# Optimization experiments

Measured on AMD Instinct MI355X. Metric: run time of the kernel, lower is better.

The kernel has to match this reference:

```python
import jax, jax.numpy as jnp
import numpy as np

B, T, D, H = 128, 256, 64, 512
MISSING = 128.0  # MISSING_VALUE marker from AJ-RNN repo


def _lstm_params(key, in_dim):
    k1, k2 = jax.random.split(key)
    K = jax.random.normal(k1, (in_dim, 4 * H), jnp.float32) * 0.05
    R = jax.random.normal(k2, (H, 4 * H), jnp.float32) * 0.05
    # Keras LSTMCell: zeros bias with unit forget bias (gate order i, f, c, o)
    b = jnp.concatenate([jnp.zeros((H,)), jnp.ones((H,)), jnp.zeros((2 * H,))]).astype(jnp.float32)
    return K, R, b


def setup_inputs() -> dict:
    key = jax.random.key(0)
    ks = jax.random.split(key, 6)
    x = jax.random.normal(ks[0], (B, T, D), jnp.float32)
    miss = jax.random.uniform(ks[1], (B, T, D)) < 0.2
    x = jnp.where(miss, MISSING, x)  # inject missing-value markers
    k0, r0, b0 = _lstm_params(ks[2], D)   # layer 0: input dim D
    k1, r1, b1 = _lstm_params(ks[3], H)   # layer 1: input dim H
    W = jax.random.normal(ks[4], (H, D), jnp.float32) * 0.1  # imputation kernel
    bias = jnp.full((D,), 0.1, jnp.float32)
    return dict(x=x, k0=k0, r0=r0, b0=b0, k1=k1, r1=r1, b1=b1, W=W, bias=bias)


def _lstm_cell(x, h, c, K, R, b):
    z = x @ K + h @ R + b  # [B, 4H]
    i, f, g, o = jnp.split(z, 4, axis=-1)
    i = jax.nn.sigmoid(i)
    f = jax.nn.sigmoid(f)
    g = jnp.tanh(g)
    o = jax.nn.sigmoid(o)
    c_new = f * c + i * g
    h_new = o * jnp.tanh(c_new)
    return h_new, c_new


def reference(x, k0, r0, b0, k1, r1, b1, W, bias):
    xs = jnp.swapaxes(x, 0, 1)          # [T, B, D]
    flags = jnp.arange(T) > 0           # t==0 uses raw input, no imputation

    def step(carry, inp):
        h1, c1, h2, c2 = carry
        x_t, flag = inp
        pred = h2 @ W + bias            # prediction from previous top-layer output
        cur = jnp.where(flag & (x_t == MISSING), pred, x_t)
        h1, c1 = _lstm_cell(cur, h1, c1, k0, r0, b0)
        h2, c2 = _lstm_cell(h1, h2, c2, k1, r1, b1)
        return (h1, c1, h2, c2), h2

    init = tuple(jnp.zeros((B, H), jnp.float32) for _ in range(4))
    _, outs = jax.lax.scan(step, init, (xs, flags))  # outs: [T, B, H]

    # tf.concat(outputs[:-1], axis=1) then reshape [-1, H] == batch-major, time inner
    hidden = jnp.swapaxes(outs[:-1], 0, 1).reshape(-1, H)  # [B*(T-1), H]
    prediction = hidden @ W + bias                          # [B*(T-1), D]
    last_cell = outs[-1]                                    # [B, H]
    return prediction, last_cell
```

## Files before the change

### kernel.cpp

```cpp
#include <hip/hip_runtime.h>
#include <hip/hip_bf16.h>


typedef __bf16        v8bf  __attribute__((ext_vector_type(8)));
typedef float         f32x4 __attribute__((ext_vector_type(4)));
typedef unsigned int  u32x4 __attribute__((ext_vector_type(4)));

constexpr int B_ = 128, T_ = 256, D_ = 64, H_ = 512;

constexpr size_t OFF_WP1 = 0;
constexpr size_t OFF_WP2 = 2359296;
constexpr size_t OFF_WPP = 6553600;
constexpr size_t OFF_H1G = 6619136;
constexpr size_t OFF_H2G = 6750208;
constexpr size_t OFF_FLG = 6881280;

__device__ __forceinline__ v8bf ldv(const __hip_bfloat16* p) {
  return *reinterpret_cast<const v8bf*>(p);
}
__device__ __forceinline__ f32x4 MF(v8bf a, v8bf b, f32x4 c) {
  return __builtin_amdgcn_mfma_f32_16x16x32_bf16(a, b, c, 0, 0, 0);
}
__device__ __forceinline__ float sigf(float x) { return 1.0f / (1.0f + __expf(-x)); }
__device__ __forceinline__ float tanhfast(float x) {
  x = fminf(15.0f, fmaxf(-15.0f, x));
  float e = __expf(-2.0f * x);
  return (1.0f - e) / (1.0f + e);
}

__device__ __forceinline__ void st_llc_u16(void* p, unsigned v) {
  asm volatile("global_store_short %0, %1, off sc0 sc1" :: "v"(p), "v"(v) : "memory");
}
__device__ __forceinline__ void vm0() {
  asm volatile("s_waitcnt vmcnt(0)" ::: "memory");
}
__device__ __forceinline__ void ld_llc64_issue(const char* g, u32x4& a, u32x4& b,
                                               u32x4& c, u32x4& d) {
  asm volatile(
      "global_load_dwordx4 %0, %4, off sc0 sc1\n\t"
      "global_load_dwordx4 %1, %4, off offset:16 sc0 sc1\n\t"
      "global_load_dwordx4 %2, %4, off offset:32 sc0 sc1\n\t"
      "global_load_dwordx4 %3, %4, off offset:48 sc0 sc1"
      : "=&v"(a), "=&v"(b), "=&v"(c), "=&v"(d)
      : "v"(g)
      : "memory");
}

__global__ __launch_bounds__(256) void pack_weights(
    const float* __restrict__ kp, const float* __restrict__ rp,
    int krows, int ncols, int nkc, int nct, __hip_bfloat16* __restrict__ out) {
  int tid = blockIdx.x * 256 + threadIdx.x;
  int total = nct * nkc * 64;
  if (tid >= total) return;
  int L  = tid & 63;
  int kc = (tid >> 6) % nkc;
  int ct = tid / (64 * nkc);
  int n  = ct * 16 + (L & 15);
  int kb = kc * 32 + (L >> 4) * 8;
  __hip_bfloat16* dst = out + (size_t)tid * 8;
#pragma unroll
  for (int j = 0; j < 8; ++j) {
    int kk = kb + j;
    float v = (kk < krows) ? kp[kk * ncols + n] : rp[(kk - krows) * ncols + n];
    dst[j] = __float2bfloat16(v);
  }
}

__global__ __launch_bounds__(256) void init_state(unsigned* __restrict__ flg) {
  int idx = blockIdx.x * 256 + threadIdx.x;
  if (idx < 512) flg[idx] = 0u;
}

__global__ __launch_bounds__(256, 1) void rnn_persist(
    const float* __restrict__ x,
    const __hip_bfloat16* __restrict__ Wp1,
    const __hip_bfloat16* __restrict__ Wp2,
    const __hip_bfloat16* __restrict__ WpP,
    const float* __restrict__ b0,
    const float* __restrict__ b1,
    const float* __restrict__ biasD,
    __hip_bfloat16* __restrict__ h1g,
    __hip_bfloat16* __restrict__ h2g,
    unsigned* __restrict__ flg,
    float* __restrict__ pred_out,
    float* __restrict__ last_out) {

  __shared__ alignas(16) __hip_bfloat16 h1P[16][512];
  __shared__ alignas(16) __hip_bfloat16 h1Q[16][512];
  __shared__ alignas(16) __hip_bfloat16 h2L[16][512];
  __shared__ alignas(16) __hip_bfloat16 curL[16][72];
  __shared__ alignas(16) float predb[16][68];
  __shared__ float zb[4][16][17];

  const int tid = threadIdx.x;
  const int rg = blockIdx.x & 7;
  const int cg = blockIdx.x >> 3;
  const int w  = tid >> 6;
  const int L  = tid & 63;
  const int m  = L & 15;
  const int q  = L >> 4;
  const int row2 = tid >> 4;
  const int col2 = tid & 15;
  const int C  = cg * 16 + col2;
  const int R  = rg * 16 + row2;
  const int c0 = col2 * 4;
  const int sw = (m & 7) << 3;

  const int so0 = col2 * 64;
  const int ssw = (row2 & 7) << 4;
  const size_t gso = (size_t)row2 * 1024 + so0;

  v8bf wpp[16], wp1[18], wp2[32];
  {
    const int ct = w * 32 + cg;
#pragma unroll
    for (int kc = 0; kc < 16; ++kc)
      wpp[kc] = ldv(WpP + ((size_t)(w * 16 + kc) * 64 + L) * 8);
#pragma unroll
    for (int kc = 0; kc < 18; ++kc)
      wp1[kc] = ldv(Wp1 + ((size_t)(ct * 18 + kc) * 64 + L) * 8);
#pragma unroll
    for (int kc = 0; kc < 32; ++kc)
      wp2[kc] = ldv(Wp2 + ((size_t)(ct * 32 + kc) * 64 + L) * 8);
  }
  const float b0i = b0[C], b0f = b0[512 + C], b0g = b0[1024 + C], b0o = b0[1536 + C];
  const float b1i = b1[C], b1f = b1[512 + C], b1g = b1[1024 + C], b1o = b1[1536 + C];
  const float bD  = biasD[w * 16 + m];

  float c1v = 0.0f, c2v = 0.0f;

  const size_t rgbase = (size_t)rg * 16 * H_;
  const float* xrow = x + (size_t)R * T_ * D_;
  float* prow = pred_out + (size_t)R * (T_ - 1) * D_;
  unsigned* cnt = flg + rg * 64;
  const int hidx = R * H_ + C;

  {
    u32x4 zz = {0u, 0u, 0u, 0u};
    u32x4* p1 = reinterpret_cast<u32x4*>(&h1P[0][0]);
    u32x4* p2 = reinterpret_cast<u32x4*>(&h2L[0][0]);
#pragma unroll
    for (int i = 0; i < 4; ++i) { p1[tid * 4 + i] = zz; p2[tid * 4 + i] = zz; }
  }
  __syncthreads();

  f32x4 z1a = {0.f,0.f,0.f,0.f}, z1b = {0.f,0.f,0.f,0.f};

  for (int t = 0; t < T_; ++t) {
    __hip_bfloat16 (*h1L)[512] = (t & 1) ? h1Q : h1P;
    __hip_bfloat16 (*h1N)[512] = (t & 1) ? h1P : h1Q;

    const float4 xv = *reinterpret_cast<const float4*>(xrow + t * D_ + c0);

#pragma unroll
    for (int c = 8; c < 12; c += 2) {
      v8bf a0 = ldv(&h1L[m][(c * 32 + q * 8) ^ sw]);
      v8bf a1 = ldv(&h1L[m][((c + 1) * 32 + q * 8) ^ sw]);
      z1a = MF(a0, wp1[2 + c], z1a);
      z1b = MF(a1, wp1[3 + c], z1b);
    }
    if (t > 0 && tid < 64) {
      const unsigned tgt = 64u * (unsigned)t;
      while (__hip_atomic_load(cnt, __ATOMIC_RELAXED, __HIP_MEMORY_SCOPE_AGENT) < tgt)
        __builtin_amdgcn_s_sleep(1);
    }
    __syncthreads();

    u32x4 sa, sb, sc2, sd;
    if (t > 0)
      ld_llc64_issue((const char*)(h2g + rgbase) + gso, sa, sb, sc2, sd);
#pragma unroll
    for (int c = 12; c < 16; c += 2) {
      v8bf a0 = ldv(&h1L[m][(c * 32 + q * 8) ^ sw]);
      v8bf a1 = ldv(&h1L[m][((c + 1) * 32 + q * 8) ^ sw]);
      z1a = MF(a0, wp1[2 + c], z1a);
      z1b = MF(a1, wp1[3 + c], z1b);
    }
    if (t > 0) {
      vm0();
      char* lb = (char*)(&h2L[row2][0]);
      *(u32x4*)(lb + ((so0 +  0) ^ ssw)) = sa;
      *(u32x4*)(lb + ((so0 + 16) ^ ssw)) = sb;
      *(u32x4*)(lb + ((so0 + 32) ^ ssw)) = sc2;
      *(u32x4*)(lb + ((so0 + 48) ^ ssw)) = sd;
    }
    __syncthreads();

    if (t > 0) {
      f32x4 a0 = {0.f,0.f,0.f,0.f}, a1 = {0.f,0.f,0.f,0.f};
#pragma unroll
      for (int kc = 0; kc < 16; kc += 2) {
        v8bf x0 = ldv(&h2L[m][(kc * 32 + q * 8) ^ sw]);
        v8bf x1 = ldv(&h2L[m][((kc + 1) * 32 + q * 8) ^ sw]);
        a0 = MF(x0, wpp[kc], a0);
        a1 = MF(x1, wpp[kc + 1], a1);
      }
      a0 += a1;
#pragma unroll
      for (int r = 0; r < 4; ++r) predb[q * 4 + r][w * 16 + m] = a0[r] + bD;
    }
    __syncthreads();

    {
      float4 pv = {0.f, 0.f, 0.f, 0.f};
      if (t > 0) pv = *reinterpret_cast<const float4*>(&predb[row2][c0]);
      const float xa[4] = {xv.x, xv.y, xv.z, xv.w};
      const float pa[4] = {pv.x, pv.y, pv.z, pv.w};
#pragma unroll
      for (int j = 0; j < 4; ++j) {
        const bool missv = (t > 0) && (xa[j] == 128.0f);
        curL[row2][c0 + j] = __float2bfloat16(missv ? pa[j] : xa[j]);
      }
      if (cg == 0 && t > 0)
        *reinterpret_cast<float4*>(prow + (size_t)(t - 1) * D_ + c0) = pv;
    }
    __syncthreads();

    {
      v8bf a0 = ldv(&curL[m][q * 8]);
      v8bf a1 = ldv(&curL[m][32 + q * 8]);
      z1a = MF(a0, wp1[0], z1a);
      z1b = MF(a1, wp1[1], z1b);
      f32x4 zf = z1a + z1b;
#pragma unroll
      for (int r = 0; r < 4; ++r) zb[w][q * 4 + r][m] = zf[r];
    }
    __syncthreads();

    f32x4 z2a = {0.f,0.f,0.f,0.f}, z2b = {0.f,0.f,0.f,0.f};
    {
      float iv = zb[0][row2][col2] + b0i;
      float fv = zb[1][row2][col2] + b0f;
      float gv = zb[2][row2][col2] + b0g;
      float ov = zb[3][row2][col2] + b0o;
      float ig = sigf(iv), fg = sigf(fv), gg = tanhfast(gv), og = sigf(ov);
      c1v = fg * c1v + ig * gg;
      float hn = og * tanhfast(c1v);
      st_llc_u16(&h1g[hidx], (unsigned)__builtin_bit_cast(unsigned short,
                                                          __float2bfloat16(hn)));
    }
#pragma unroll
    for (int c = 0; c < 8; c += 2) {
      v8bf a0 = ldv(&h2L[m][(c * 32 + q * 8) ^ sw]);
      v8bf a1 = ldv(&h2L[m][((c + 1) * 32 + q * 8) ^ sw]);
      z2a = MF(a0, wp2[16 + c], z2a);
      z2b = MF(a1, wp2[17 + c], z2b);
    }
    vm0();
    __syncthreads();
    if (tid == 0)
      __hip_atomic_fetch_add(cnt, 1u, __ATOMIC_RELAXED, __HIP_MEMORY_SCOPE_AGENT);

#pragma unroll
    for (int c = 8; c < 12; c += 2) {
      v8bf a0 = ldv(&h2L[m][(c * 32 + q * 8) ^ sw]);
      v8bf a1 = ldv(&h2L[m][((c + 1) * 32 + q * 8) ^ sw]);
      z2a = MF(a0, wp2[16 + c], z2a);
      z2b = MF(a1, wp2[17 + c], z2b);
    }
    if (tid < 64) {
      const unsigned tgt = 32u * (2u * (unsigned)t + 1u);
      while (__hip_atomic_load(cnt, __ATOMIC_RELAXED, __HIP_MEMORY_SCOPE_AGENT) < tgt)
        __builtin_amdgcn_s_sleep(1);
    }
    __syncthreads();

    ld_llc64_issue((const char*)(h1g + rgbase) + gso, sa, sb, sc2, sd);
#pragma unroll
    for (int c = 12; c < 16; c += 2) {
      v8bf a0 = ldv(&h2L[m][(c * 32 + q * 8) ^ sw]);
      v8bf a1 = ldv(&h2L[m][((c + 1) * 32 + q * 8) ^ sw]);
      z2a = MF(a0, wp2[16 + c], z2a);
      z2b = MF(a1, wp2[17 + c], z2b);
    }
    vm0();
    {
      char* lb = (char*)(&h1N[row2][0]);
      *(u32x4*)(lb + ((so0 +  0) ^ ssw)) = sa;
      *(u32x4*)(lb + ((so0 + 16) ^ ssw)) = sb;
      *(u32x4*)(lb + ((so0 + 32) ^ ssw)) = sc2;
      *(u32x4*)(lb + ((so0 + 48) ^ ssw)) = sd;
    }
    __syncthreads();

    {
#pragma unroll
      for (int c = 0; c < 16; c += 2) {
        v8bf a0 = ldv(&h1N[m][(c * 32 + q * 8) ^ sw]);
        v8bf a1 = ldv(&h1N[m][((c + 1) * 32 + q * 8) ^ sw]);
        z2a = MF(a0, wp2[c], z2a);
        z2b = MF(a1, wp2[c + 1], z2b);
      }
      f32x4 zf = z2a + z2b;
#pragma unroll
      for (int r = 0; r < 4; ++r) zb[w][q * 4 + r][m] = zf[r];
    }
    __syncthreads();

    {
      float iv = zb[0][row2][col2] + b1i;
      float fv = zb[1][row2][col2] + b1f;
      float gv = zb[2][row2][col2] + b1g;
      float ov = zb[3][row2][col2] + b1o;
      float ig = sigf(iv), fg = sigf(fv), gg = tanhfast(gv), og = sigf(ov);
      c2v = fg * c2v + ig * gg;
      float hn = og * tanhfast(c2v);
      if (t == T_ - 1) {
        last_out[hidx] = hn;
        break;
      }
      st_llc_u16(&h2g[hidx], (unsigned)__builtin_bit_cast(unsigned short,
                                                          __float2bfloat16(hn)));
    }
    z1a = (f32x4){0.f,0.f,0.f,0.f};
    z1b = (f32x4){0.f,0.f,0.f,0.f};
#pragma unroll
    for (int c = 0; c < 8; c += 2) {
      v8bf a0 = ldv(&h1N[m][(c * 32 + q * 8) ^ sw]);
      v8bf a1 = ldv(&h1N[m][((c + 1) * 32 + q * 8) ^ sw]);
      z1a = MF(a0, wp1[2 + c], z1a);
      z1b = MF(a1, wp1[3 + c], z1b);
    }
    vm0();
    __syncthreads();
    if (tid == 0)
      __hip_atomic_fetch_add(cnt, 1u, __ATOMIC_RELAXED, __HIP_MEMORY_SCOPE_AGENT);
  }
}

extern "C" void kernel_launch(void* const* d_in, const int* in_sizes, int n_in,
                              void* d_out, int out_size, void* d_ws, size_t ws_size,
                              hipStream_t stream) {
  const float* x    = (const float*)d_in[0];
  const float* k0   = (const float*)d_in[1];
  const float* r0   = (const float*)d_in[2];
  const float* b0   = (const float*)d_in[3];
  const float* k1   = (const float*)d_in[4];
  const float* r1   = (const float*)d_in[5];
  const float* b1   = (const float*)d_in[6];
  const float* W    = (const float*)d_in[7];
  const float* bias = (const float*)d_in[8];

  char* ws = (char*)d_ws;
  __hip_bfloat16* Wp1 = (__hip_bfloat16*)(ws + OFF_WP1);
  __hip_bfloat16* Wp2 = (__hip_bfloat16*)(ws + OFF_WP2);
  __hip_bfloat16* WpP = (__hip_bfloat16*)(ws + OFF_WPP);
  __hip_bfloat16* h1g = (__hip_bfloat16*)(ws + OFF_H1G);
  __hip_bfloat16* h2g = (__hip_bfloat16*)(ws + OFF_H2G);
  unsigned*       flg = (unsigned*)(ws + OFF_FLG);

  pack_weights<<<(128 * 18 * 64 + 255) / 256, 256, 0, stream>>>(k0, r0, 64, 2048, 18, 128, Wp1);
  pack_weights<<<(128 * 32 * 64 + 255) / 256, 256, 0, stream>>>(k1, r1, 512, 2048, 32, 128, Wp2);
  pack_weights<<<(4 * 16 * 64 + 255) / 256, 256, 0, stream>>>(W, W, 512, 64, 16, 4, WpP);
  init_state<<<2, 256, 0, stream>>>(flg);

  float* outp = (float*)d_out;
  float* last = outp + (size_t)B_ * (T_ - 1) * D_;

  rnn_persist<<<256, 256, 0, stream>>>(x, Wp1, Wp2, WpP, b0, b1, bias,
                                       h1g, h2g, flg, outp, last);
}
```

Baseline: 1.467 ms.

## Interleave two batch row-groups per block to hide inter-block sync latency

```diff
diff --git a/kernel.cpp b/kernel.cpp
--- a/kernel.cpp
+++ b/kernel.cpp
@@ -69,6 +69,198 @@
 __global__ __launch_bounds__(256) void init_state(unsigned* __restrict__ flg) {
   int idx = blockIdx.x * 256 + threadIdx.x;
   if (idx < 512) flg[idx] = 0u;
+}
+
+struct TC {
+  int tid, cg, w, m, q, row2, col2, c0, sw, so0, ssw;
+  size_t gso;
+};
+
+__device__ __forceinline__ void half1(
+    int t, const TC& tc,
+    __hip_bfloat16 (*h1L)[512], __hip_bfloat16 (*h2L)[512],
+    __hip_bfloat16 (*curL)[72], float (*predb)[68], float (*zb)[16][17],
+    unsigned* cnt, const float* xrow, float* prow,
+    const char* h2src, __hip_bfloat16* h1dst,
+    const v8bf (&wpp)[16], const v8bf (&wp1)[18],
+    float b0i, float b0f, float b0g, float b0o, float bD,
+    float& c1v) {
+  const int tid = tc.tid, m = tc.m, q = tc.q, w = tc.w;
+  const int row2 = tc.row2, col2 = tc.col2, c0 = tc.c0, sw = tc.sw;
+  const int so0 = tc.so0, ssw = tc.ssw;
+  f32x4 z1a = {0.f,0.f,0.f,0.f}, z1b = {0.f,0.f,0.f,0.f};
+  const float4 xv = *reinterpret_cast<const float4*>(xrow + t * D_ + c0);
+
+  if (t > 0) {
+    if (tid < 64) {
+      const unsigned tgt = 64u * (unsigned)t;
+      while (__hip_atomic_load(cnt, __ATOMIC_RELAXED, __HIP_MEMORY_SCOPE_AGENT) < tgt)
+        __builtin_amdgcn_s_sleep(1);
+    }
+    __syncthreads();
+    u32x4 sa, sb, sc2, sd;
+    ld_llc64_issue(h2src + tc.gso, sa, sb, sc2, sd);
+#pragma unroll
+    for (int c = 0; c < 8; c += 2) {
+      v8bf a0 = ldv(&h1L[m][(c * 32 + q * 8) ^ sw]);
+      v8bf a1 = ldv(&h1L[m][((c + 1) * 32 + q * 8) ^ sw]);
+      z1a = MF(a0, wp1[2 + c], z1a);
+      z1b = MF(a1, wp1[3 + c], z1b);
+    }
+    vm0();
+    {
+      char* lb = (char*)(&h2L[row2][0]);
+      *(u32x4*)(lb + ((so0 +  0) ^ ssw)) = sa;
+      *(u32x4*)(lb + ((so0 + 16) ^ ssw)) = sb;
+      *(u32x4*)(lb + ((so0 + 32) ^ ssw)) = sc2;
+      *(u32x4*)(lb + ((so0 + 48) ^ ssw)) = sd;
+    }
+    __syncthreads();
+    {
+      f32x4 a0 = {0.f,0.f,0.f,0.f}, a1 = {0.f,0.f,0.f,0.f};
+#pragma unroll
+      for (int kc = 0; kc < 16; kc += 2) {
+        v8bf x0 = ldv(&h2L[m][(kc * 32 + q * 8) ^ sw]);
+        v8bf x1 = ldv(&h2L[m][((kc + 1) * 32 + q * 8) ^ sw]);
+        a0 = MF(x0, wpp[kc], a0);
+        a1 = MF(x1, wpp[kc + 1], a1);
+      }
+      a0 += a1;
+#pragma unroll
+      for (int r = 0; r < 4; ++r) predb[q * 4 + r][w * 16 + m] = a0[r] + bD;
+    }
+    __syncthreads();
+  }
+
+  {
+    float4 pv = {0.f, 0.f, 0.f, 0.f};
+    if (t > 0) pv = *reinterpret_cast<const float4*>(&predb[row2][c0]);
+    const float xa[4] = {xv.x, xv.y, xv.z, xv.w};
+    const float pa[4] = {pv.x, pv.y, pv.z, pv.w};
+#pragma unroll
+    for (int j = 0; j < 4; ++j) {
+      const bool missv = (t > 0) && (xa[j] == 128.0f);
+      curL[row2][c0 + j] = __float2bfloat16(missv ? pa[j] : xa[j]);
+    }
+    if (tc.cg == 0 && t > 0)
+      *reinterpret_cast<float4*>(prow + (size_t)(t - 1) * D_ + c0) = pv;
+  }
+  __syncthreads();
+
+  {
+#pragma unroll
+    for (int c = 8; c < 16; c += 2) {
+      v8bf a0 = ldv(&h1L[m][(c * 32 + q * 8) ^ sw]);
+      v8bf a1 = ldv(&h1L[m][((c + 1) * 32 + q * 8) ^ sw]);
+      z1a = MF(a0, wp1[2 + c], z1a);
+      z1b = MF(a1, wp1[3 + c], z1b);
+    }
+    v8bf a0 = ldv(&curL[m][q * 8]);
+    v8bf a1 = ldv(&curL[m][32 + q * 8]);
+    z1a = MF(a0, wp1[0], z1a);
+    z1b = MF(a1, wp1[1], z1b);
+    f32x4 zf = z1a + z1b;
+#pragma unroll
+    for (int r = 0; r < 4; ++r) zb[w][q * 4 + r][m] = zf[r];
+  }
+  __syncthreads();
+
+  {
+    float iv = zb[0][row2][col2] + b0i;
+    float fv = zb[1][row2][col2] + b0f;
+    float gv = zb[2][row2][col2] + b0g;
+    float ov = zb[3][row2][col2] + b0o;
+    float ig = sigf(iv), fg = sigf(fv), gg = tanhfast(gv), og = sigf(ov);
+    c1v = fg * c1v + ig * gg;
+    float hn = og * tanhfast(c1v);
+    st_llc_u16(h1dst, (unsigned)__builtin_bit_cast(unsigned short,
+                                                   __float2bfloat16(hn)));
+  }
+  vm0();
+  __syncthreads();
+  if (tid == 0)
+    __hip_atomic_fetch_add(cnt, 1u, __ATOMIC_RELAXED, __HIP_MEMORY_SCOPE_AGENT);
+}
+
+__device__ __forceinline__ void half2(
+    int t, const TC& tc,
+    __hip_bfloat16 (*h1N)[512], __hip_bfloat16 (*h2L)[512],
+    float (*zb)[16][17],
+    unsigned* cnt, const char* h1src,
+    __hip_bfloat16* h2dst, float* lastp,
+    const v8bf (&wp2)[32],
+    float b1i, float b1f, float b1g, float b1o,
+    float& c2v) {
+  const int tid = tc.tid, m = tc.m, q = tc.q, w = tc.w;
+  const int row2 = tc.row2, col2 = tc.col2, sw = tc.sw;
+  const int so0 = tc.so0, ssw = tc.ssw;
+  f32x4 z2a = {0.f,0.f,0.f,0.f}, z2b = {0.f,0.f,0.f,0.f};
+
+#pragma unroll
+  for (int c = 0; c < 8; c += 2) {
+    v8bf a0 = ldv(&h2L[m][(c * 32 + q * 8) ^ sw]);
+    v8bf a1 = ldv(&h2L[m][((c + 1) * 32 + q * 8) ^ sw]);
+    z2a = MF(a0, wp2[16 + c], z2a);
+    z2b = MF(a1, wp2[17 + c], z2b);
+  }
+  if (tid < 64) {
+    const unsigned tgt = 32u * (2u * (unsigned)t + 1u);
+    while (__hip_atomic_load(cnt, __ATOMIC_RELAXED, __HIP_MEMORY_SCOPE_AGENT) < tgt)
+      __builtin_amdgcn_s_sleep(1);
+  }
+  __syncthreads();
+  {
+    u32x4 sa, sb, sc2, sd;
+    ld_llc64_issue(h1src + tc.gso, sa, sb, sc2, sd);
+#pragma unroll
+    for (int c = 8; c < 16; c += 2) {
+      v8bf a0 = ldv(&h2L[m][(c * 32 + q * 8) ^ sw]);
+      v8bf a1 = ldv(&h2L[m][((c + 1) * 32 + q * 8) ^ sw]);
+      z2a = MF(a0, wp2[16 + c], z2a);
+      z2b = MF(a1, wp2[17 + c], z2b);
+    }
+    vm0();
+    char* lb = (char*)(&h1N[row2][0]);
+    *(u32x4*)(lb + ((so0 +  0) ^ ssw)) = sa;
+    *(u32x4*)(lb + ((so0 + 16) ^ ssw)) = sb;
+    *(u32x4*)(lb + ((so0 + 32) ^ ssw)) = sc2;
+    *(u32x4*)(lb + ((so0 + 48) ^ ssw)) = sd;
+  }
+  __syncthreads();
+  {
+#pragma unroll
+    for (int c = 0; c < 16; c += 2) {
+      v8bf a0 = ldv(&h1N[m][(c * 32 + q * 8) ^ sw]);
+      v8bf a1 = ldv(&h1N[m][((c + 1) * 32 + q * 8) ^ sw]);
+      z2a = MF(a0, wp2[c], z2a);
+      z2b = MF(a1, wp2[c + 1], z2b);
+    }
+    f32x4 zf = z2a + z2b;
+#pragma unroll
+    for (int r = 0; r < 4; ++r) zb[w][q * 4 + r][m] = zf[r];
+  }
+  __syncthreads();
+  {
+    float iv = zb[0][row2][col2] + b1i;
+    float fv = zb[1][row2][col2] + b1f;
+    float gv = zb[2][row2][col2] + b1g;
+    float ov = zb[3][row2][col2] + b1o;
+    float ig = sigf(iv), fg = sigf(fv), gg = tanhfast(gv), og = sigf(ov);
+    c2v = fg * c2v + ig * gg;
+    float hn = og * tanhfast(c2v);
+    if (t == T_ - 1) {
+      *lastp = hn;
+    } else {
+      st_llc_u16(h2dst, (unsigned)__builtin_bit_cast(unsigned short,
+                                                     __float2bfloat16(hn)));
+    }
+  }
+  if (t != T_ - 1) {
+    vm0();
+    __syncthreads();
+    if (tid == 0)
+      __hip_atomic_fetch_add(cnt, 1u, __ATOMIC_RELAXED, __HIP_MEMORY_SCOPE_AGENT);
+  }
 }
 
 __global__ __launch_bounds__(256, 1) void rnn_persist(
@@ -85,37 +277,38 @@
     float* __restrict__ pred_out,
     float* __restrict__ last_out) {
 
-  __shared__ alignas(16) __hip_bfloat16 h1P[16][512];
-  __shared__ alignas(16) __hip_bfloat16 h1Q[16][512];
-  __shared__ alignas(16) __hip_bfloat16 h2L[16][512];
-  __shared__ alignas(16) __hip_bfloat16 curL[16][72];
-  __shared__ alignas(16) float predb[16][68];
-  __shared__ float zb[4][16][17];
-
-  const int tid = threadIdx.x;
-  const int rg = blockIdx.x & 7;
-  const int cg = blockIdx.x >> 3;
-  const int w  = tid >> 6;
-  const int L  = tid & 63;
-  const int m  = L & 15;
-  const int q  = L >> 4;
-  const int row2 = tid >> 4;
-  const int col2 = tid & 15;
-  const int C  = cg * 16 + col2;
-  const int R  = rg * 16 + row2;
-  const int c0 = col2 * 4;
-  const int sw = (m & 7) << 3;
-
-  const int so0 = col2 * 64;
-  const int ssw = (row2 & 7) << 4;
-  const size_t gso = (size_t)row2 * 1024 + so0;
+  __shared__ alignas(16) __hip_bfloat16 h1PA[16][512], h1QA[16][512], h2LA[16][512];
+  __shared__ alignas(16) __hip_bfloat16 h1PB[16][512], h1QB[16][512], h2LB[16][512];
+  __shared__ alignas(16) __hip_bfloat16 curLA[16][72], curLB[16][72];
+  __shared__ alignas(16) float predbA[16][68], predbB[16][68];
+  __shared__ float zbA[4][16][17], zbB[4][16][17];
+
+  TC tc;
+  tc.tid  = threadIdx.x;
+  const int pr = blockIdx.x & 3;
+  tc.cg   = blockIdx.x >> 2;
+  tc.w    = tc.tid >> 6;
+  const int L = tc.tid & 63;
+  tc.m    = L & 15;
+  tc.q    = L >> 4;
+  tc.row2 = tc.tid >> 4;
+  tc.col2 = tc.tid & 15;
+  tc.c0   = tc.col2 * 4;
+  tc.sw   = (tc.m & 7) << 3;
+  tc.so0  = tc.col2 * 64;
+  tc.ssw  = (tc.row2 & 7) << 4;
+  tc.gso  = (size_t)tc.row2 * 1024 + tc.so0;
+
+  const int rgA = pr, rgB = pr + 4;
+  const int C = tc.cg * 16 + tc.col2;
+  const int RA = rgA * 16 + tc.row2, RB = rgB * 16 + tc.row2;
 
   v8bf wpp[16], wp1[18], wp2[32];
   {
-    const int ct = w * 32 + cg;
+    const int ct = tc.w * 32 + tc.cg;
 #pragma unroll
     for (int kc = 0; kc < 16; ++kc)
-      wpp[kc] = ldv(WpP + ((size_t)(w * 16 + kc) * 64 + L) * 8);
+      wpp[kc] = ldv(WpP + ((size_t)(tc.w * 16 + kc) * 64 + L) * 8);
 #pragma unroll
     for (int kc = 0; kc < 18; ++kc)
       wp1[kc] = ldv(Wp1 + ((size_t)(ct * 18 + kc) * 64 + L) * 8);
@@ -125,206 +318,51 @@
   }
   const float b0i = b0[C], b0f = b0[512 + C], b0g = b0[1024 + C], b0o = b0[1536 + C];
   const float b1i = b1[C], b1f = b1[512 + C], b1g = b1[1024 + C], b1o = b1[1536 + C];
-  const float bD  = biasD[w * 16 + m];
-
-  float c1v = 0.0f, c2v = 0.0f;
-
-  const size_t rgbase = (size_t)rg * 16 * H_;
-  const float* xrow = x + (size_t)R * T_ * D_;
-  float* prow = pred_out + (size_t)R * (T_ - 1) * D_;
-  unsigned* cnt = flg + rg * 64;
-  const int hidx = R * H_ + C;
+  const float bD  = biasD[tc.w * 16 + tc.m];
+
+  float c1A = 0.0f, c2A = 0.0f, c1B = 0.0f, c2B = 0.0f;
+
+  const size_t rgbaseA = (size_t)rgA * 16 * H_, rgbaseB = (size_t)rgB * 16 * H_;
+  const float* xrowA = x + (size_t)RA * T_ * D_;
+  const float* xrowB = x + (size_t)RB * T_ * D_;
+  float* prowA = pred_out + (size_t)RA * (T_ - 1) * D_;
+  float* prowB = pred_out + (size_t)RB * (T_ - 1) * D_;
+  unsigned* cntA = flg + rgA * 64;
+  unsigned* cntB = flg + rgB * 64;
+  const int hidxA = RA * H_ + C, hidxB = RB * H_ + C;
+  const char* h2srcA = (const char*)(h2g + rgbaseA);
+  const char* h2srcB = (const char*)(h2g + rgbaseB);
+  const char* h1srcA = (const char*)(h1g + rgbaseA);
+  const char* h1srcB = (const char*)(h1g + rgbaseB);
 
   {
     u32x4 zz = {0u, 0u, 0u, 0u};
-    u32x4* p1 = reinterpret_cast<u32x4*>(&h1P[0][0]);
-    u32x4* p2 = reinterpret_cast<u32x4*>(&h2L[0][0]);
-#pragma unroll
-    for (int i = 0; i < 4; ++i) { p1[tid * 4 + i] = zz; p2[tid * 4 + i] = zz; }
-  }
-  __syncthreads();
-
-  f32x4 z1a = {0.f,0.f,0.f,0.f}, z1b = {0.f,0.f,0.f,0.f};
+    u32x4* p1 = reinterpret_cast<u32x4*>(&h1PA[0][0]);
+    u32x4* p2 = reinterpret_cast<u32x4*>(&h2LA[0][0]);
+    u32x4* p3 = reinterpret_cast<u32x4*>(&h1PB[0][0]);
+    u32x4* p4 = reinterpret_cast<u32x4*>(&h2LB[0][0]);
+#pragma unroll
+    for (int i = 0; i < 4; ++i) {
+      p1[tc.tid * 4 + i] = zz; p2[tc.tid * 4 + i] = zz;
+      p3[tc.tid * 4 + i] = zz; p4[tc.tid * 4 + i] = zz;
+    }
+  }
+  __syncthreads();
 
   for (int t = 0; t < T_; ++t) {
-    __hip_bfloat16 (*h1L)[512] = (t & 1) ? h1Q : h1P;
-    __hip_bfloat16 (*h1N)[512] = (t & 1) ? h1P : h1Q;
-
-    const float4 xv = *reinterpret_cast<const float4*>(xrow + t * D_ + c0);
-
-#pragma unroll
-    for (int c = 8; c < 12; c += 2) {
-      v8bf a0 = ldv(&h1L[m][(c * 32 + q * 8) ^ sw]);
-      v8bf a1 = ldv(&h1L[m][((c + 1) * 32 + q * 8) ^ sw]);
-      z1a = MF(a0, wp1[2 + c], z1a);
-      z1b = MF(a1, wp1[3 + c], z1b);
-    }
-    if (t > 0 && tid < 64) {
-      const unsigned tgt = 64u * (unsigned)t;
-      while (__hip_atomic_load(cnt, __ATOMIC_RELAXED, __HIP_MEMORY_SCOPE_AGENT) < tgt)
-        __builtin_amdgcn_s_sleep(1);
-    }
-    __syncthreads();
-
-    u32x4 sa, sb, sc2, sd;
-    if (t > 0)
-      ld_llc64_issue((const char*)(h2g + rgbase) + gso, sa, sb, sc2, sd);
-#pragma unroll
-    for (int c = 12; c < 16; c += 2) {
-      v8bf a0 = ldv(&h1L[m][(c * 32 + q * 8) ^ sw]);
-      v8bf a1 = ldv(&h1L[m][((c + 1) * 32 + q * 8) ^ sw]);
-      z1a = MF(a0, wp1[2 + c], z1a);
-      z1b = MF(a1, wp1[3 + c], z1b);
-    }
-    if (t > 0) {
-      vm0();
-      char* lb = (char*)(&h2L[row2][0]);
-      *(u32x4*)(lb + ((so0 +  0) ^ ssw)) = sa;
-      *(u32x4*)(lb + ((so0 + 16) ^ ssw)) = sb;
-      *(u32x4*)(lb + ((so0 + 32) ^ ssw)) = sc2;
-      *(u32x4*)(lb + ((so0 + 48) ^ ssw)) = sd;
-    }
-    __syncthreads();
-
-    if (t > 0) {
-      f32x4 a0 = {0.f,0.f,0.f,0.f}, a1 = {0.f,0.f,0.f,0.f};
-#pragma unroll
-      for (int kc = 0; kc < 16; kc += 2) {
-        v8bf x0 = ldv(&h2L[m][(kc * 32 + q * 8) ^ sw]);
-        v8bf x1 = ldv(&h2L[m][((kc + 1) * 32 + q * 8) ^ sw]);
-        a0 = MF(x0, wpp[kc], a0);
-        a1 = MF(x1, wpp[kc + 1], a1);
-      }
-      a0 += a1;
-#pragma unroll
-      for (int r = 0; r < 4; ++r) predb[q * 4 + r][w * 16 + m] = a0[r] + bD;
-    }
-    __syncthreads();
-
-    {
-      float4 pv = {0.f, 0.f, 0.f, 0.f};
-      if (t > 0) pv = *reinterpret_cast<const float4*>(&predb[row2][c0]);
-      const float xa[4] = {xv.x, xv.y, xv.z, xv.w};
-      const float pa[4] = {pv.x, pv.y, pv.z, pv.w};
-#pragma unroll
-      for (int j = 0; j < 4; ++j) {
-        const bool missv = (t > 0) && (xa[j] == 128.0f);
-        curL[row2][c0 + j] = __float2bfloat16(missv ? pa[j] : xa[j]);
-      }
-      if (cg == 0 && t > 0)
-        *reinterpret_cast<float4*>(prow + (size_t)(t - 1) * D_ + c0) = pv;
-    }
-    __syncthreads();
-
-    {
-      v8bf a0 = ldv(&curL[m][q * 8]);
-      v8bf a1 = ldv(&curL[m][32 + q * 8]);
-      z1a = MF(a0, wp1[0], z1a);
-      z1b = MF(a1, wp1[1], z1b);
-      f32x4 zf = z1a + z1b;
-#pragma unroll
-      for (int r = 0; r < 4; ++r) zb[w][q * 4 + r][m] = zf[r];
-    }
-    __syncthreads();
-
-    f32x4 z2a = {0.f,0.f,0.f,0.f}, z2b = {0.f,0.f,0.f,0.f};
-    {
-      float iv = zb[0][row2][col2] + b0i;
-      float fv = zb[1][row2][col2] + b0f;
-      float gv = zb[2][row2][col2] + b0g;
-      float ov = zb[3][row2][col2] + b0o;
-      float ig = sigf(iv), fg = sigf(fv), gg = tanhfast(gv), og = sigf(ov);
-      c1v = fg * c1v + ig * gg;
-      float hn = og * tanhfast(c1v);
-      st_llc_u16(&h1g[hidx], (unsigned)__builtin_bit_cast(unsigned short,
-                                                          __float2bfloat16(hn)));
-    }
-#pragma unroll
-    for (int c = 0; c < 8; c += 2) {
-      v8bf a0 = ldv(&h2L[m][(c * 32 + q * 8) ^ sw]);
-      v8bf a1 = ldv(&h2L[m][((c + 1) * 32 + q * 8) ^ sw]);
-      z2a = MF(a0, wp2[16 + c], z2a);
-      z2b = MF(a1, wp2[17 + c], z2b);
-    }
-    vm0();
-    __syncthreads();
-    if (tid == 0)
-      __hip_atomic_fetch_add(cnt, 1u, __ATOMIC_RELAXED, __HIP_MEMORY_SCOPE_AGENT);
-
-#pragma unroll
-    for (int c = 8; c < 12; c += 2) {
-      v8bf a0 = ldv(&h2L[m][(c * 32 + q * 8) ^ sw]);
-      v8bf a1 = ldv(&h2L[m][((c + 1) * 32 + q * 8) ^ sw]);
-      z2a = MF(a0, wp2[16 + c], z2a);
-      z2b = MF(a1, wp2[17 + c], z2b);
-    }
-    if (tid < 64) {
-      const unsigned tgt = 32u * (2u * (unsigned)t + 1u);
-      while (__hip_atomic_load(cnt, __ATOMIC_RELAXED, __HIP_MEMORY_SCOPE_AGENT) < tgt)
-        __builtin_amdgcn_s_sleep(1);
-    }
-    __syncthreads();
-
-    ld_llc64_issue((const char*)(h1g + rgbase) + gso, sa, sb, sc2, sd);
-#pragma unroll
-    for (int c = 12; c < 16; c += 2) {
-      v8bf a0 = ldv(&h2L[m][(c * 32 + q * 8) ^ sw]);
-      v8bf a1 = ldv(&h2L[m][((c + 1) * 32 + q * 8) ^ sw]);
-      z2a = MF(a0, wp2[16 + c], z2a);
-      z2b = MF(a1, wp2[17 + c], z2b);
-    }
-    vm0();
-    {
-      char* lb = (char*)(&h1N[row2][0]);
-      *(u32x4*)(lb + ((so0 +  0) ^ ssw)) = sa;
-      *(u32x4*)(lb + ((so0 + 16) ^ ssw)) = sb;
-      *(u32x4*)(lb + ((so0 + 32) ^ ssw)) = sc2;
-      *(u32x4*)(lb + ((so0 + 48) ^ ssw)) = sd;
-    }
-    __syncthreads();
-
-    {
-#pragma unroll
-      for (int c = 0; c < 16; c += 2) {
-        v8bf a0 = ldv(&h1N[m][(c * 32 + q * 8) ^ sw]);
-        v8bf a1 = ldv(&h1N[m][((c + 1) * 32 + q * 8) ^ sw]);
-        z2a = MF(a0, wp2[c], z2a);
-        z2b = MF(a1, wp2[c + 1], z2b);
-      }
-      f32x4 zf = z2a + z2b;
-#pragma unroll
-      for (int r = 0; r < 4; ++r) zb[w][q * 4 + r][m] = zf[r];
-    }
-    __syncthreads();
-
-    {
-      float iv = zb[0][row2][col2] + b1i;
-      float fv = zb[1][row2][col2] + b1f;
-      float gv = zb[2][row2][col2] + b1g;
-      float ov = zb[3][row2][col2] + b1o;
-      float ig = sigf(iv), fg = sigf(fv), gg = tanhfast(gv), og = sigf(ov);
-      c2v = fg * c2v + ig * gg;
-      float hn = og * tanhfast(c2v);
-      if (t == T_ - 1) {
-        last_out[hidx] = hn;
-        break;
-      }
-      st_llc_u16(&h2g[hidx], (unsigned)__builtin_bit_cast(unsigned short,
-                                                          __float2bfloat16(hn)));
-    }
-    z1a = (f32x4){0.f,0.f,0.f,0.f};
-    z1b = (f32x4){0.f,0.f,0.f,0.f};
-#pragma unroll
-    for (int c = 0; c < 8; c += 2) {
-      v8bf a0 = ldv(&h1N[m][(c * 32 + q * 8) ^ sw]);
-      v8bf a1 = ldv(&h1N[m][((c + 1) * 32 + q * 8) ^ sw]);
-      z1a = MF(a0, wp1[2 + c], z1a);
-      z1b = MF(a1, wp1[3 + c], z1b);
-    }
-    vm0();
-    __syncthreads();
-    if (tid == 0)
-      __hip_atomic_fetch_add(cnt, 1u, __ATOMIC_RELAXED, __HIP_MEMORY_SCOPE_AGENT);
+    __hip_bfloat16 (*h1LA)[512] = (t & 1) ? h1QA : h1PA;
+    __hip_bfloat16 (*h1NA)[512] = (t & 1) ? h1PA : h1QA;
+    __hip_bfloat16 (*h1LB)[512] = (t & 1) ? h1QB : h1PB;
+    __hip_bfloat16 (*h1NB)[512] = (t & 1) ? h1PB : h1QB;
+
+    half1(t, tc, h1LA, h2LA, curLA, predbA, zbA, cntA, xrowA, prowA,
+          h2srcA, h1g + hidxA, wpp, wp1, b0i, b0f, b0g, b0o, bD, c1A);
+    half1(t, tc, h1LB, h2LB, curLB, predbB, zbB, cntB, xrowB, prowB,
+          h2srcB, h1g + hidxB, wpp, wp1, b0i, b0f, b0g, b0o, bD, c1B);
+    half2(t, tc, h1NA, h2LA, zbA, cntA, h1srcA,
+          h2g + hidxA, last_out + hidxA, wp2, b1i, b1f, b1g, b1o, c2A);
+    half2(t, tc, h1NB, h2LB, zbB, cntB, h1srcB,
+          h2g + hidxB, last_out + hidxB, wp2, b1i, b1f, b1g, b1o, c2B);
   }
 }
 
@@ -357,6 +395,6 @@
   float* outp = (float*)d_out;
   float* last = outp + (size_t)B_ * (T_ - 1) * D_;
 
-  rnn_persist<<<256, 256, 0, stream>>>(x, Wp1, Wp2, WpP, b0, b1, bias,
+  rnn_persist<<<128, 256, 0, stream>>>(x, Wp1, Wp2, WpP, b0, b1, bias,
                                        h1g, h2g, flg, outp, last);
 }
```

After: 2.628 ms. 79.1% more time.
